# Kernel tuning notes

Measured on AMD Instinct MI355X. Metric: run time of the kernel, lower is better.

The kernel has to match this reference:

```python
import jax, jax.numpy as jnp
import numpy as np

N = 65536
APP = 1024
SP = 512
HID = 512
CARD = 16
SUB = HID // CARD  # 32


def setup_inputs() -> dict:
    key = jax.random.key(0)
    ks = jax.random.split(key, 8)
    s1 = 1.0 / np.sqrt(APP)
    s2 = 1.0 / np.sqrt(SP)
    s3 = 1.0 / np.sqrt(SUB)
    return {
        "appearance": jax.random.normal(ks[0], (N, APP), jnp.float32),
        "spatial": jax.random.normal(ks[1], (N, SP), jnp.float32),
        # Batched per-branch weights (torch Linear: y = x @ W.T + b; here stored as [in, out])
        "W1": jax.random.uniform(ks[2], (CARD, APP, SUB), jnp.float32, -s1, s1),
        "b1": jax.random.uniform(ks[3], (CARD, SUB), jnp.float32, -s1, s1),
        "W2": jax.random.uniform(ks[4], (CARD, SP, SUB), jnp.float32, -s2, s2),
        "b2": jax.random.uniform(ks[5], (CARD, SP if False else SUB), jnp.float32, -s2, s2),
        "W3": jax.random.uniform(ks[6], (CARD, SUB, HID), jnp.float32, -s3, s3),
        "b3": jax.random.uniform(ks[7], (CARD, HID), jnp.float32, -s3, s3),
    }


def reference(appearance, spatial, W1, b1, W2, b2, W3, b3):
    # fc1[c] = appearance @ W1[c] + b1[c]; fc2[c] = spatial @ W2[c] + b2[c]
    h1 = jnp.einsum('na,cas->ncs', appearance, W1) + b1[None]  # [N, C, SUB]
    h2 = jnp.einsum('np,cps->ncs', spatial, W2) + b2[None]     # [N, C, SUB]
    h = jax.nn.relu(h1 + h2)
    # sum over branches of (h[:,c] @ W3[c] + b3[c]) == einsum + sum of biases
    out = jnp.einsum('ncs,csh->nh', h, W3) + jnp.sum(b3, axis=0)[None]  # [N, HID]
    return jax.nn.relu(out)
```

## Files before the change

### kernel.cpp

```cpp
#include <hip/hip_runtime.h>

typedef __attribute__((ext_vector_type(4))) float floatx4;
typedef __attribute__((ext_vector_type(8))) short bf16x8;

__device__ __forceinline__ unsigned short f2bf(float f) {
    union { float f; unsigned u; } v; v.f = f;
    unsigned r = v.u + 0x7fffu + ((v.u >> 16) & 1u);
    return (unsigned short)(r >> 16);
}

__global__ void prep_kernel(const float* __restrict__ W1, const float* __restrict__ b1,
                            const float* __restrict__ W2, const float* __restrict__ b2,
                            const float* __restrict__ W3, const float* __restrict__ b3,
                            unsigned short* __restrict__ wcat, unsigned short* __restrict__ w3f,
                            float* __restrict__ bias12, float* __restrict__ bias3s)
{
    int tid = blockIdx.x * 256 + threadIdx.x;
    if (tid < 98304) {
        int l  = tid & 63;
        int nt = (tid >> 6) & 31;
        int kc = tid >> 11;
        int n  = nt * 16 + (l & 15);
        int k0 = kc * 32 + ((l >> 4) << 3);
        int c = n >> 5, s = n & 31;
        union { unsigned short us[8]; int4 v; } pk;
        const float* src = (k0 < 1024) ? (W1 + c * 32768 + k0 * 32 + s)
                                       : (W2 + c * 16384 + (k0 - 1024) * 32 + s);
        #pragma unroll
        for (int j = 0; j < 8; ++j) pk.us[j] = f2bf(src[j * 32]);
        *(int4*)(wcat + (size_t)tid * 8) = pk.v;
    } else if (tid < 131072) {
        int t  = tid - 98304;
        int l  = t & 63;
        int nt = (t >> 6) & 31;
        int kc = t >> 11;
        int n  = nt * 16 + (l & 15);
        int k0 = kc * 32 + ((l >> 4) << 3);
        union { unsigned short us[8]; int4 v; } pk;
        const float* src = W3 + k0 * 512 + n;
        #pragma unroll
        for (int j = 0; j < 8; ++j) pk.us[j] = f2bf(src[j * 512]);
        *(int4*)(w3f + (size_t)t * 8) = pk.v;
    } else if (tid < 131584) {
        int n = tid - 131072;
        bias12[n] = b1[n] + b2[n];
        float sacc = 0.f;
        #pragma unroll
        for (int c = 0; c < 16; ++c) sacc += b3[c * 512 + n];
        bias3s[n] = sacc;
    }
}

__global__ __launch_bounds__(256, 2) void fused_main(
    const float* __restrict__ app, const float* __restrict__ sp,
    const unsigned short* __restrict__ wcat, const unsigned short* __restrict__ w3f,
    const float* __restrict__ bias12, const float* __restrict__ bias3s,
    float* __restrict__ out)
{
    __shared__ unsigned short As[2][4][64][8];
    __shared__ unsigned short Hf[4][16][64][8];

    const int tid = (int)threadIdx.x;
    const int w   = tid >> 6;
    const int l   = tid & 63;
    const int rowbase = (int)blockIdx.x * 64;

    const int sr  = tid >> 2;
    const int scc = tid & 3;
    const float* appsrc = app + (size_t)(rowbase + sr) * 1024 + scc * 8;
    const float* spsrc  = sp  + (size_t)(rowbase + sr) * 512  + scc * 8;
    unsigned short* as0 = &As[0][sr >> 4][scc * 16 + (sr & 15)][0];
    unsigned short* as1 = &As[1][sr >> 4][scc * 16 + (sr & 15)][0];

    floatx4 acc[4][8];
    #pragma unroll
    for (int mt = 0; mt < 4; ++mt)
        #pragma unroll
        for (int nt = 0; nt < 8; ++nt)
            acc[mt][nt] = (floatx4){0.f, 0.f, 0.f, 0.f};

    {
        float4 p0 = *(const float4*)(appsrc);
        float4 p1 = *(const float4*)(appsrc + 4);
        union { unsigned short us[8]; int4 v; } pk;
        pk.us[0] = f2bf(p0.x); pk.us[1] = f2bf(p0.y); pk.us[2] = f2bf(p0.z); pk.us[3] = f2bf(p0.w);
        pk.us[4] = f2bf(p1.x); pk.us[5] = f2bf(p1.y); pk.us[6] = f2bf(p1.z); pk.us[7] = f2bf(p1.w);
        *(int4*)as0 = pk.v;
    }

    for (int kb = 0; kb < 48; ++kb) {
        __syncthreads();
        const int buf = kb & 1;
        float4 p0, p1;
        if (kb + 1 < 48) {
            const float* src = (kb + 1 < 32) ? (appsrc + (kb + 1) * 32)
                                             : (spsrc + (kb + 1 - 32) * 32);
            p0 = *(const float4*)(src);
            p1 = *(const float4*)(src + 4);
        }
        bf16x8 bfrag[8];
        #pragma unroll
        for (int nt = 0; nt < 8; ++nt)
            bfrag[nt] = *(const bf16x8*)(wcat + (((size_t)kb * 32 + w * 8 + nt) * 64 + l) * 8);
        bf16x8 afrag[4];
        #pragma unroll
        for (int mt = 0; mt < 4; ++mt)
            afrag[mt] = *(const bf16x8*)(&As[buf][mt][l][0]);
        #pragma unroll
        for (int mt = 0; mt < 4; ++mt)
            #pragma unroll
            for (int nt = 0; nt < 8; ++nt)
                acc[mt][nt] = __builtin_amdgcn_mfma_f32_16x16x32_bf16(
                    afrag[mt], bfrag[nt], acc[mt][nt], 0, 0, 0);
        if (kb + 1 < 48) {
            union { unsigned short us[8]; int4 v; } pk;
            pk.us[0] = f2bf(p0.x); pk.us[1] = f2bf(p0.y); pk.us[2] = f2bf(p0.z); pk.us[3] = f2bf(p0.w);
            pk.us[4] = f2bf(p1.x); pk.us[5] = f2bf(p1.y); pk.us[6] = f2bf(p1.z); pk.us[7] = f2bf(p1.w);
            *(int4*)((buf == 0) ? as1 : as0) = pk.v;
        }
    }

    #pragma unroll
    for (int nt = 0; nt < 8; ++nt) {
        const int colg = w * 128 + nt * 16 + (l & 15);
        const float bv = bias12[colg];
        const int kc  = colg >> 5;
        const int lhi = ((colg >> 3) & 3) << 4;
        const int j   = colg & 7;
        #pragma unroll
        for (int mt = 0; mt < 4; ++mt)
            #pragma unroll
            for (int r = 0; r < 4; ++r) {
                const int rlow = ((l >> 4) << 2) + r;
                float v = acc[mt][nt][r] + bv;
                v = fmaxf(v, 0.f);
                Hf[mt][kc][lhi + rlow][j] = f2bf(v);
            }
    }
    __syncthreads();

    #pragma unroll
    for (int mt = 0; mt < 4; ++mt)
        #pragma unroll
        for (int nt = 0; nt < 8; ++nt)
            acc[mt][nt] = (floatx4){0.f, 0.f, 0.f, 0.f};

    for (int kc = 0; kc < 16; ++kc) {
        bf16x8 bfrag[8];
        #pragma unroll
        for (int nt = 0; nt < 8; ++nt)
            bfrag[nt] = *(const bf16x8*)(w3f + (((size_t)kc * 32 + w * 8 + nt) * 64 + l) * 8);
        bf16x8 afrag[4];
        #pragma unroll
        for (int mt = 0; mt < 4; ++mt)
            afrag[mt] = *(const bf16x8*)(&Hf[mt][kc][l][0]);
        #pragma unroll
        for (int mt = 0; mt < 4; ++mt)
            #pragma unroll
            for (int nt = 0; nt < 8; ++nt)
                acc[mt][nt] = __builtin_amdgcn_mfma_f32_16x16x32_bf16(
                    afrag[mt], bfrag[nt], acc[mt][nt], 0, 0, 0);
    }

    #pragma unroll
    for (int nt = 0; nt < 8; ++nt) {
        const int colg = w * 128 + nt * 16 + (l & 15);
        const float bv = bias3s[colg];
        #pragma unroll
        for (int mt = 0; mt < 4; ++mt)
            #pragma unroll
            for (int r = 0; r < 4; ++r) {
                const int rowg = mt * 16 + ((l >> 4) << 2) + r;
                float v = acc[mt][nt][r] + bv;
                v = fmaxf(v, 0.f);
                out[(size_t)(rowbase + rowg) * 512 + colg] = v;
            }
    }
}

extern "C" void kernel_launch(void* const* d_in, const int* in_sizes, int n_in,
                              void* d_out, int out_size, void* d_ws, size_t ws_size,
                              hipStream_t stream)
{
    const float* app = (const float*)d_in[0];
    const float* sp  = (const float*)d_in[1];
    const float* W1  = (const float*)d_in[2];
    const float* b1  = (const float*)d_in[3];
    const float* W2  = (const float*)d_in[4];
    const float* b2  = (const float*)d_in[5];
    const float* W3  = (const float*)d_in[6];
    const float* b3  = (const float*)d_in[7];

    char* ws = (char*)d_ws;
    unsigned short* wcat  = (unsigned short*)(ws);
    unsigned short* w3f   = (unsigned short*)(ws + 1572864);
    float*          b12   = (float*)(ws + 2097152);
    float*          b3s   = (float*)(ws + 2099200);

    prep_kernel<<<514, 256, 0, stream>>>(W1, b1, W2, b2, W3, b3, wcat, w3f, b12, b3s);

    float* outp = (float*)d_out;
    fused_main<<<65536 / 64, 256, 0, stream>>>(app, sp, wcat, w3f, b12, b3s, outp);
}
```

Before: 586.0 us.

## Load activation fragments directly from global, drop LDS staging and barriers

```diff
diff --git a/kernel.cpp b/kernel.cpp
--- a/kernel.cpp
+++ b/kernel.cpp
@@ -57,20 +57,17 @@
     const float* __restrict__ bias12, const float* __restrict__ bias3s,
     float* __restrict__ out)
 {
-    __shared__ unsigned short As[2][4][64][8];
     __shared__ unsigned short Hf[4][16][64][8];
 
     const int tid = (int)threadIdx.x;
     const int w   = tid >> 6;
     const int l   = tid & 63;
+    const int lm  = l & 15;
+    const int klo = l >> 4;
     const int rowbase = (int)blockIdx.x * 64;
 
-    const int sr  = tid >> 2;
-    const int scc = tid & 3;
-    const float* appsrc = app + (size_t)(rowbase + sr) * 1024 + scc * 8;
-    const float* spsrc  = sp  + (size_t)(rowbase + sr) * 512  + scc * 8;
-    unsigned short* as0 = &As[0][sr >> 4][scc * 16 + (sr & 15)][0];
-    unsigned short* as1 = &As[1][sr >> 4][scc * 16 + (sr & 15)][0];
+    const float* baseA = app + (size_t)(rowbase + lm) * 1024 + klo * 8;
+    const float* baseS = sp  + (size_t)(rowbase + lm) * 512  + klo * 8;
 
     floatx4 acc[4][8];
     #pragma unroll
@@ -79,45 +76,48 @@
         for (int nt = 0; nt < 8; ++nt)
             acc[mt][nt] = (floatx4){0.f, 0.f, 0.f, 0.f};
 
-    {
-        float4 p0 = *(const float4*)(appsrc);
-        float4 p1 = *(const float4*)(appsrc + 4);
-        union { unsigned short us[8]; int4 v; } pk;
-        pk.us[0] = f2bf(p0.x); pk.us[1] = f2bf(p0.y); pk.us[2] = f2bf(p0.z); pk.us[3] = f2bf(p0.w);
-        pk.us[4] = f2bf(p1.x); pk.us[5] = f2bf(p1.y); pk.us[6] = f2bf(p1.z); pk.us[7] = f2bf(p1.w);
-        *(int4*)as0 = pk.v;
+    float4 pa0[4], pa1[4];
+    #pragma unroll
+    for (int mt = 0; mt < 4; ++mt) {
+        const float* s = baseA + mt * 16384;
+        pa0[mt] = *(const float4*)s;
+        pa1[mt] = *(const float4*)(s + 4);
     }
 
     for (int kb = 0; kb < 48; ++kb) {
-        __syncthreads();
-        const int buf = kb & 1;
-        float4 p0, p1;
+        bf16x8 bfrag[8];
+        #pragma unroll
+        for (int nt = 0; nt < 8; ++nt)
+            bfrag[nt] = *(const bf16x8*)(wcat + (((size_t)kb * 32 + w * 8 + nt) * 64 + l) * 8);
+
+        bf16x8 afrag[4];
+        #pragma unroll
+        for (int mt = 0; mt < 4; ++mt) {
+            union { unsigned short us[8]; bf16x8 v; } pk;
+            pk.us[0] = f2bf(pa0[mt].x); pk.us[1] = f2bf(pa0[mt].y);
+            pk.us[2] = f2bf(pa0[mt].z); pk.us[3] = f2bf(pa0[mt].w);
+            pk.us[4] = f2bf(pa1[mt].x); pk.us[5] = f2bf(pa1[mt].y);
+            pk.us[6] = f2bf(pa1[mt].z); pk.us[7] = f2bf(pa1[mt].w);
+            afrag[mt] = pk.v;
+        }
+
         if (kb + 1 < 48) {
-            const float* src = (kb + 1 < 32) ? (appsrc + (kb + 1) * 32)
-                                             : (spsrc + (kb + 1 - 32) * 32);
-            p0 = *(const float4*)(src);
-            p1 = *(const float4*)(src + 4);
+            const int kn = kb + 1;
+            #pragma unroll
+            for (int mt = 0; mt < 4; ++mt) {
+                const float* s = (kn < 32) ? (baseA + mt * 16384 + kn * 32)
+                                           : (baseS + mt * 8192 + (kn - 32) * 32);
+                pa0[mt] = *(const float4*)s;
+                pa1[mt] = *(const float4*)(s + 4);
+            }
         }
-        bf16x8 bfrag[8];
-        #pragma unroll
-        for (int nt = 0; nt < 8; ++nt)
-            bfrag[nt] = *(const bf16x8*)(wcat + (((size_t)kb * 32 + w * 8 + nt) * 64 + l) * 8);
-        bf16x8 afrag[4];
-        #pragma unroll
-        for (int mt = 0; mt < 4; ++mt)
-            afrag[mt] = *(const bf16x8*)(&As[buf][mt][l][0]);
+
         #pragma unroll
         for (int mt = 0; mt < 4; ++mt)
             #pragma unroll
             for (int nt = 0; nt < 8; ++nt)
                 acc[mt][nt] = __builtin_amdgcn_mfma_f32_16x16x32_bf16(
                     afrag[mt], bfrag[nt], acc[mt][nt], 0, 0, 0);
-        if (kb + 1 < 48) {
-            union { unsigned short us[8]; int4 v; } pk;
-            pk.us[0] = f2bf(p0.x); pk.us[1] = f2bf(p0.y); pk.us[2] = f2bf(p0.z); pk.us[3] = f2bf(p0.w);
-            pk.us[4] = f2bf(p1.x); pk.us[5] = f2bf(p1.y); pk.us[6] = f2bf(p1.z); pk.us[7] = f2bf(p1.w);
-            *(int4*)((buf == 0) ? as1 : as0) = pk.v;
-        }
     }
 
     #pragma unroll
```

New measurement: 642.6 us. 1.1x slower.

## Split fused MLP into two GEMM kernels with HBM intermediate and 32-row tiles

Applied to the files above, without the earlier changes.

```diff
diff --git a/kernel.cpp b/kernel.cpp
--- a/kernel.cpp
+++ b/kernel.cpp
@@ -51,13 +51,170 @@
     }
 }
 
+__global__ __launch_bounds__(256, 3) void k1_gemm(
+    const float* __restrict__ app, const float* __restrict__ sp,
+    const unsigned short* __restrict__ wcat, const float* __restrict__ bias12,
+    unsigned short* __restrict__ hblob)
+{
+    __shared__ unsigned short As[4][2][2][64][8];
+
+    const int tid = (int)threadIdx.x;
+    const int w   = tid >> 6;
+    const int l   = tid & 63;
+    const int r8  = l >> 3;
+    const int kq  = l & 7;
+    const int rowbase = (int)blockIdx.x * 32;
+
+    const float* srcA[4];
+    const float* srcS[4];
+    #pragma unroll
+    for (int i = 0; i < 4; ++i) {
+        srcA[i] = app + (size_t)(rowbase + i * 8 + r8) * 1024 + kq * 4;
+        srcS[i] = sp  + (size_t)(rowbase + i * 8 + r8) * 512  + kq * 4;
+    }
+    const int dmt[4] = {0, 0, 1, 1};
+    int dlane[4], dj = (kq & 1) * 4;
+    #pragma unroll
+    for (int i = 0; i < 4; ++i) dlane[i] = (kq >> 1) * 16 + (i & 1) * 8 + r8;
+
+    floatx4 acc[2][8];
+    #pragma unroll
+    for (int mt = 0; mt < 2; ++mt)
+        #pragma unroll
+        for (int nt = 0; nt < 8; ++nt)
+            acc[mt][nt] = (floatx4){0.f, 0.f, 0.f, 0.f};
+
+    float4 pa[4];
+    #pragma unroll
+    for (int i = 0; i < 4; ++i) pa[i] = *(const float4*)(srcA[i]);
+    #pragma unroll
+    for (int i = 0; i < 4; ++i) {
+        union { unsigned short us[4]; unsigned long long u; } pk;
+        pk.us[0] = f2bf(pa[i].x); pk.us[1] = f2bf(pa[i].y);
+        pk.us[2] = f2bf(pa[i].z); pk.us[3] = f2bf(pa[i].w);
+        *(unsigned long long*)&As[w][0][dmt[i]][dlane[i]][dj] = pk.u;
+    }
+    #pragma unroll
+    for (int i = 0; i < 4; ++i) pa[i] = *(const float4*)(srcA[i] + 32);
+
+    for (int kb = 0; kb < 48; ++kb) {
+        const int buf = kb & 1;
+        bf16x8 bfrag[8];
+        #pragma unroll
+        for (int nt = 0; nt < 8; ++nt)
+            bfrag[nt] = *(const bf16x8*)(wcat + (((size_t)kb * 32 + w * 8 + nt) * 64 + l) * 8);
+        bf16x8 afrag[2];
+        #pragma unroll
+        for (int mt = 0; mt < 2; ++mt)
+            afrag[mt] = *(const bf16x8*)(&As[w][buf][mt][l][0]);
+        if (kb + 1 < 48) {
+            #pragma unroll
+            for (int i = 0; i < 4; ++i) {
+                union { unsigned short us[4]; unsigned long long u; } pk;
+                pk.us[0] = f2bf(pa[i].x); pk.us[1] = f2bf(pa[i].y);
+                pk.us[2] = f2bf(pa[i].z); pk.us[3] = f2bf(pa[i].w);
+                *(unsigned long long*)&As[w][buf ^ 1][dmt[i]][dlane[i]][dj] = pk.u;
+            }
+        }
+        if (kb + 2 < 48) {
+            const int kn = kb + 2;
+            #pragma unroll
+            for (int i = 0; i < 4; ++i)
+                pa[i] = (kn < 32) ? *(const float4*)(srcA[i] + kn * 32)
+                                  : *(const float4*)(srcS[i] + (kn - 32) * 32);
+        }
+        #pragma unroll
+        for (int mt = 0; mt < 2; ++mt)
+            #pragma unroll
+            for (int nt = 0; nt < 8; ++nt)
+                acc[mt][nt] = __builtin_amdgcn_mfma_f32_16x16x32_bf16(
+                    afrag[mt], bfrag[nt], acc[mt][nt], 0, 0, 0);
+    }
+
+    #pragma unroll
+    for (int nt = 0; nt < 8; ++nt) {
+        const int colg = w * 128 + nt * 16 + (l & 15);
+        const float bv = bias12[colg];
+        const int kc = colg >> 5;
+        const int kl = (colg >> 3) & 3;
+        const int j  = colg & 7;
+        #pragma unroll
+        for (int mt = 0; mt < 2; ++mt) {
+            size_t base = (((size_t)blockIdx.x * 2 + mt) * 16 + kc) * 512 + (size_t)kl * 128 + j;
+            #pragma unroll
+            for (int r = 0; r < 4; ++r) {
+                float v = fmaxf(acc[mt][nt][r] + bv, 0.f);
+                hblob[base + (size_t)(((l >> 4) << 2) + r) * 8] = f2bf(v);
+            }
+        }
+    }
+}
+
+__global__ __launch_bounds__(256, 3) void k2_gemm(
+    const unsigned short* __restrict__ hblob, const unsigned short* __restrict__ w3f,
+    const float* __restrict__ bias3s, float* __restrict__ out)
+{
+    const int tid = (int)threadIdx.x;
+    const int w   = tid >> 6;
+    const int l   = tid & 63;
+    const int tile = (int)blockIdx.x;
+    const int rowbase = tile * 32;
+
+    floatx4 acc[2][8];
+    #pragma unroll
+    for (int mt = 0; mt < 2; ++mt)
+        #pragma unroll
+        for (int nt = 0; nt < 8; ++nt)
+            acc[mt][nt] = (floatx4){0.f, 0.f, 0.f, 0.f};
+
+    const unsigned short* hbase = hblob + (size_t)tile * 2 * 16 * 512 + (size_t)l * 8;
+    bf16x8 paf[2];
+    #pragma unroll
+    for (int mt = 0; mt < 2; ++mt)
+        paf[mt] = *(const bf16x8*)(hbase + (size_t)mt * 16 * 512);
+
+    for (int kc = 0; kc < 16; ++kc) {
+        bf16x8 bfrag[8];
+        #pragma unroll
+        for (int nt = 0; nt < 8; ++nt)
+            bfrag[nt] = *(const bf16x8*)(w3f + (((size_t)kc * 32 + w * 8 + nt) * 64 + l) * 8);
+        bf16x8 afrag[2];
+        afrag[0] = paf[0]; afrag[1] = paf[1];
+        if (kc + 1 < 16) {
+            #pragma unroll
+            for (int mt = 0; mt < 2; ++mt)
+                paf[mt] = *(const bf16x8*)(hbase + ((size_t)mt * 16 + (kc + 1)) * 512);
+        }
+        #pragma unroll
+        for (int mt = 0; mt < 2; ++mt)
+            #pragma unroll
+            for (int nt = 0; nt < 8; ++nt)
+                acc[mt][nt] = __builtin_amdgcn_mfma_f32_16x16x32_bf16(
+                    afrag[mt], bfrag[nt], acc[mt][nt], 0, 0, 0);
+    }
+
+    #pragma unroll
+    for (int nt = 0; nt < 8; ++nt) {
+        const int colg = w * 128 + nt * 16 + (l & 15);
+        const float bv = bias3s[colg];
+        #pragma unroll
+        for (int mt = 0; mt < 2; ++mt)
+            #pragma unroll
+            for (int r = 0; r < 4; ++r) {
+                const int rowg = mt * 16 + ((l >> 4) << 2) + r;
+                float v = fmaxf(acc[mt][nt][r] + bv, 0.f);
+                out[(size_t)(rowbase + rowg) * 512 + colg] = v;
+            }
+    }
+}
+
 __global__ __launch_bounds__(256, 2) void fused_main(
     const float* __restrict__ app, const float* __restrict__ sp,
     const unsigned short* __restrict__ wcat, const unsigned short* __restrict__ w3f,
     const float* __restrict__ bias12, const float* __restrict__ bias3s,
     float* __restrict__ out)
 {
-    __shared__ unsigned short As[2][4][64][8];
+    __shared__ unsigned short AsF[2][4][64][8];
     __shared__ unsigned short Hf[4][16][64][8];
 
     const int tid = (int)threadIdx.x;
@@ -69,8 +226,8 @@
     const int scc = tid & 3;
     const float* appsrc = app + (size_t)(rowbase + sr) * 1024 + scc * 8;
     const float* spsrc  = sp  + (size_t)(rowbase + sr) * 512  + scc * 8;
-    unsigned short* as0 = &As[0][sr >> 4][scc * 16 + (sr & 15)][0];
-    unsigned short* as1 = &As[1][sr >> 4][scc * 16 + (sr & 15)][0];
+    unsigned short* as0 = &AsF[0][sr >> 4][scc * 16 + (sr & 15)][0];
+    unsigned short* as1 = &AsF[1][sr >> 4][scc * 16 + (sr & 15)][0];
 
     floatx4 acc[4][8];
     #pragma unroll
@@ -105,7 +262,7 @@
         bf16x8 afrag[4];
         #pragma unroll
         for (int mt = 0; mt < 4; ++mt)
-            afrag[mt] = *(const bf16x8*)(&As[buf][mt][l][0]);
+            afrag[mt] = *(const bf16x8*)(&AsF[buf][mt][l][0]);
         #pragma unroll
         for (int mt = 0; mt < 4; ++mt)
             #pragma unroll
@@ -132,8 +289,7 @@
             #pragma unroll
             for (int r = 0; r < 4; ++r) {
                 const int rlow = ((l >> 4) << 2) + r;
-                float v = acc[mt][nt][r] + bv;
-                v = fmaxf(v, 0.f);
+                float v = fmaxf(acc[mt][nt][r] + bv, 0.f);
                 Hf[mt][kc][lhi + rlow][j] = f2bf(v);
             }
     }
@@ -171,8 +327,7 @@
             #pragma unroll
             for (int r = 0; r < 4; ++r) {
                 const int rowg = mt * 16 + ((l >> 4) << 2) + r;
-                float v = acc[mt][nt][r] + bv;
-                v = fmaxf(v, 0.f);
+                float v = fmaxf(acc[mt][nt][r] + bv, 0.f);
                 out[(size_t)(rowbase + rowg) * 512 + colg] = v;
             }
     }
@@ -196,9 +351,15 @@
     unsigned short* w3f   = (unsigned short*)(ws + 1572864);
     float*          b12   = (float*)(ws + 2097152);
     float*          b3s   = (float*)(ws + 2099200);
+    unsigned short* hblob = (unsigned short*)(ws + 4194304);
 
     prep_kernel<<<514, 256, 0, stream>>>(W1, b1, W2, b2, W3, b3, wcat, w3f, b12, b3s);
 
     float* outp = (float*)d_out;
-    fused_main<<<65536 / 64, 256, 0, stream>>>(app, sp, wcat, w3f, b12, b3s, outp);
-}
+    if (ws_size >= (size_t)4194304 + 67108864) {
+        k1_gemm<<<2048, 256, 0, stream>>>(app, sp, wcat, b12, hblob);
+        k2_gemm<<<2048, 256, 0, stream>>>(hblob, w3f, b3s, outp);
+    } else {
+        fused_main<<<1024, 256, 0, stream>>>(app, sp, wcat, w3f, b12, b3s, outp);
+    }
+}
```

Result: slower. 738.9 us (+26.1%).
